# Kernel optimization log

Measured on AMD Instinct MI355X. Metric: run time of the kernel, lower is better.

## Reference

```python
import jax, jax.numpy as jnp
import numpy as np

B, S, H, DH = 4, 2048, 16, 64
D = H * DH          # 1024
EXP = 2
FF_IN = EXP * D * 2  # 4096 (SwiGLU doubles)
FF_HID = EXP * D     # 2048
SCALE_BASE = 512
LN_EPS = 1e-5


def setup_inputs() -> dict:
    key = jax.random.key(0)
    ks = jax.random.split(key, 8)
    inp = {
        "q": jax.random.normal(ks[0], (B, S, D), jnp.float32),
        "k": jax.random.normal(ks[1], (B, S, D), jnp.float32),
        "v": jax.random.normal(ks[2], (B, S, D), jnp.float32),
        "Wqkv": jax.random.normal(ks[3], (D, 3 * D), jnp.float32) * (1.0 / np.sqrt(D)),
        "bqkv": jnp.zeros((3 * D,), jnp.float32),
        "q_scale": jnp.ones((DH,), jnp.float32),
        "k_scale": jnp.ones((DH,), jnp.float32),
        "ln_g": jnp.ones((D,), jnp.float32),
        "ln_b": jnp.zeros((D,), jnp.float32),
        "W1": jax.random.normal(ks[4], (D, FF_IN), jnp.float32) * (1.0 / np.sqrt(D)),
        "b1": jnp.zeros((FF_IN,), jnp.float32),
        "W2": jax.random.normal(ks[5], (FF_HID, D), jnp.float32) * (1.0 / np.sqrt(FF_HID)),
        "b2": jnp.zeros((D,), jnp.float32),
    }
    return inp


def rotate_half(x):
    x1, x2 = jnp.split(x, 2, axis=-1)
    return jnp.concatenate((-x2, x1), axis=-1)


def apply_rope(pos, t, scale):
    # pos: [S, DH], scale: [S, DH] (broadcast over [B, H, S, DH])
    return t * jnp.cos(pos) * scale + rotate_half(t) * jnp.sin(pos) * scale


def rotary_tables(seq_len):
    inv_freq = 1.0 / (10000.0 ** (jnp.arange(0, DH, 2, dtype=jnp.float32) / DH))
    t = jnp.arange(seq_len, dtype=jnp.float32)
    freqs = t[:, None] * inv_freq[None, :]            # [S, DH/2]
    freqs = jnp.concatenate((freqs, freqs), axis=-1)  # [S, DH]
    power = (t - seq_len // 2) / SCALE_BASE           # [S]
    base = (jnp.arange(0, DH, 2, dtype=jnp.float32) + 0.4 * DH) / (1.4 * DH)  # [DH/2]
    scale = base[None, :] ** power[:, None]           # [S, DH/2]
    scale = jnp.concatenate((scale, scale), axis=-1)  # [S, DH]
    return freqs, scale


def l2norm(x, eps=1e-12):
    n = jnp.sqrt(jnp.sum(x * x, axis=-1, keepdims=True))
    return x / jnp.maximum(n, eps)


def reference(q, k, v, Wqkv, bqkv, q_scale, k_scale, ln_g, ln_b, W1, b1, W2, b2):
    del k, v  # module projects qkv from q; k,v args are unused (faithful to source)
    n, seq_len, _ = q.shape
    qkv = q @ Wqkv + bqkv                              # [B, S, 3D]
    qkv = qkv.reshape(n, seq_len, H, 3 * DH).transpose(0, 2, 1, 3)  # [B, H, S, 3DH]
    q_, k_, v_ = jnp.split(qkv, 3, axis=-1)
    q_ = l2norm(q_) * q_scale
    k_ = l2norm(k_) * k_scale
    pos, xscale = rotary_tables(seq_len)
    q_ = apply_rope(pos, q_, xscale)
    k_ = apply_rope(pos, k_, 1.0 / xscale)
    # scaled dot product attention (non-causal)
    scores = jnp.einsum("bhid,bhjd->bhij", q_, k_) / np.sqrt(DH)
    attn = jax.nn.softmax(scores, axis=-1)
    out = jnp.einsum("bhij,bhjd->bhid", attn, v_)      # [B, H, S, DH]
    out = out.transpose(0, 2, 1, 3).reshape(n, seq_len, D)
    # LayerNorm
    mu = jnp.mean(out, axis=-1, keepdims=True)
    var = jnp.mean((out - mu) ** 2, axis=-1, keepdims=True)
    out = (out - mu) / jnp.sqrt(var + LN_EPS) * ln_g + ln_b
    # SwiGLU FFN (dropout = identity in eval)
    h = out @ W1 + b1                                  # [B, S, FF_IN]
    x_, gate = jnp.split(h, 2, axis=-1)
    ff = (jax.nn.silu(gate) * x_) @ W2 + b2            # [B, S, D]
    return out + ff
```

## Files before the change

kernel.cpp:

```cpp
#include <hip/hip_runtime.h>
#include <math.h>


typedef __bf16 bf16;
typedef bf16 bf16x8 __attribute__((ext_vector_type(8)));
typedef bf16 bf16x4 __attribute__((ext_vector_type(4)));
typedef float f32x4 __attribute__((ext_vector_type(4)));

#define MFMA(a, b, c) __builtin_amdgcn_mfma_f32_16x16x32_bf16(a, b, c, 0, 0, 0)

__device__ __forceinline__ void async16(const void* g, void* l) {
    __builtin_amdgcn_global_load_lds(
        (const __attribute__((address_space(1))) void*)g,
        (__attribute__((address_space(3))) void*)l,
        16, 0, 0);
}

__global__ __launch_bounds__(256) void fill_sentinel(float* __restrict__ o)
{
    size_t i = ((size_t)blockIdx.x * 256 + threadIdx.x) * 4;
    *(float4*)&o[i] = make_float4(0.25f, 0.25f, 0.25f, 0.25f);
}

__global__ __launch_bounds__(256) void transpose_f32_bf16(
    const float* __restrict__ in, bf16* __restrict__ out, int K, int N)
{
    __shared__ bf16 T[64][70];
    const int tN = N >> 6;
    const int tk = blockIdx.x / tN, tn = blockIdx.x % tN;
    const int k0 = tk << 6, n0 = tn << 6;
    const int t = threadIdx.x;
    const int r = t >> 2, c0 = (t & 3) << 4;
    const float* src = &in[(size_t)(k0 + r) * N + n0 + c0];
    for (int j = 0; j < 4; ++j) {
        float4 f = *(const float4*)(src + 4 * j);
        T[r][c0 + 4 * j + 0] = (bf16)f.x;
        T[r][c0 + 4 * j + 1] = (bf16)f.y;
        T[r][c0 + 4 * j + 2] = (bf16)f.z;
        T[r][c0 + 4 * j + 3] = (bf16)f.w;
    }
    __syncthreads();
    bf16x8 o0, o1;
    for (int i = 0; i < 8; ++i) o0[i] = T[c0 + i][r];
    for (int i = 0; i < 8; ++i) o1[i] = T[c0 + 8 + i][r];
    *(bf16x8*)&out[(size_t)(n0 + r) * K + k0 + c0]     = o0;
    *(bf16x8*)&out[(size_t)(n0 + r) * K + k0 + c0 + 8] = o1;
}

__global__ __launch_bounds__(256) void transpose_v(
    const bf16* __restrict__ in, bf16* __restrict__ out)
{
    __shared__ bf16 T[64][72];
    const int bh = blockIdx.x >> 5;
    const int s0 = (blockIdx.x & 31) << 6;
    const bf16* ip = in + ((size_t)bh << 17) + (size_t)s0 * 64;
    bf16* op = out + ((size_t)bh << 17) + s0;
    const int t = threadIdx.x;
    const int r = t >> 2, c0 = (t & 3) << 4;
    *(bf16x8*)&T[r][c0]     = *(const bf16x8*)&ip[r * 64 + c0];
    *(bf16x8*)&T[r][c0 + 8] = *(const bf16x8*)&ip[r * 64 + c0 + 8];
    __syncthreads();
    bf16x8 o0, o1;
    for (int i = 0; i < 8; ++i) o0[i] = T[c0 + i][r];
    for (int i = 0; i < 8; ++i) o1[i] = T[c0 + 8 + i][r];
    *(bf16x8*)&op[(size_t)r * 2048 + c0]     = o0;
    *(bf16x8*)&op[(size_t)r * 2048 + c0 + 8] = o1;
}

template <int EPI, bool AF32>
__global__ __launch_bounds__(256) void gemm_bt(
    const void* __restrict__ Avp, const bf16* __restrict__ BT,
    const float* __restrict__ bias, int M, int N, int K, int lda,
    bf16* __restrict__ C0, bf16* __restrict__ C1, bf16* __restrict__ C2,
    float* __restrict__ Cf, const bf16* __restrict__ resid)
{
    __shared__ bf16 As[128 * 64];
    __shared__ bf16 Bs[128 * 64];
    const int tid = threadIdx.x;
    const int lane = tid & 63, wave = tid >> 6;
    const int quad = lane >> 4, l16 = lane & 15;
    const int wm = wave >> 1, wn = wave & 1;
    const int nb = N >> 7;
    const int bm = blockIdx.x / nb, bn = blockIdx.x % nb;
    const int m0 = bm << 7, n0 = bn << 7;
    const float* Af = (const float*)Avp;
    const bf16*  Ab = (const bf16*)Avp;
    char* aB = (char*)&As[0];
    char* bB = (char*)&Bs[0];
    const int rsw = l16 & 7;

    f32x4 acc[4][4] = {};

    for (int kt = 0; kt < K; kt += 64) {
        for (int i = 0; i < 4; ++i) {
            int l = (i << 8) + tid;
            int r = l >> 3;
            int cbs = ((l & 7) ^ (r & 7)) << 3;
            int cu = (i << 8) + (wave << 6);
            if (!AF32)
                async16(&Ab[(size_t)(m0 + r) * lda + kt + cbs], aB + (size_t)cu * 16);
            async16(&BT[(size_t)(n0 + r) * K + kt + cbs], bB + (size_t)cu * 16);
        }
        if (AF32) {
            for (int i = 0; i < 4; ++i) {
                int l = (i << 8) + tid;
                int r = l >> 3;
                int cbs = ((l & 7) ^ (r & 7)) << 3;
                const float* s = &Af[(size_t)(m0 + r) * lda + kt + cbs];
                float4 f0 = *(const float4*)s;
                float4 f1 = *(const float4*)(s + 4);
                bf16x8 tv;
                tv[0] = (bf16)f0.x; tv[1] = (bf16)f0.y;
                tv[2] = (bf16)f0.z; tv[3] = (bf16)f0.w;
                tv[4] = (bf16)f1.x; tv[5] = (bf16)f1.y;
                tv[6] = (bf16)f1.z; tv[7] = (bf16)f1.w;
                *(bf16x8*)&As[l << 3] = tv;
            }
        }
        __syncthreads();
        for (int kd = 0; kd < 2; ++kd) {
            bf16x8 af[4], bfr[4];
            for (int mi = 0; mi < 4; ++mi) {
                int row = (wm << 6) + (mi << 4) + l16;
                af[mi] = *(const bf16x8*)&As[(row << 6) + ((((kd << 2) + quad) ^ rsw) << 3)];
            }
            for (int ni = 0; ni < 4; ++ni) {
                int row = (wn << 6) + (ni << 4) + l16;
                bfr[ni] = *(const bf16x8*)&Bs[(row << 6) + ((((kd << 2) + quad) ^ rsw) << 3)];
            }
            for (int mi = 0; mi < 4; ++mi)
                for (int ni = 0; ni < 4; ++ni)
                    acc[mi][ni] = MFMA(af[mi], bfr[ni], acc[mi][ni]);
        }
        __syncthreads();
    }

    for (int mi = 0; mi < 4; ++mi) {
        for (int ni = 0; ni < 4; ++ni) {
            for (int r = 0; r < 4; ++r) {
                int row = m0 + (wm << 6) + (mi << 4) + (quad << 2) + r;
                int col = n0 + (wn << 6) + (ni << 4) + l16;
                float v = acc[mi][ni][r] + bias[col];
                if (EPI == 0) {
                    int b = row >> 11, s = row & 2047;
                    int h = col / 192, w = col % 192;
                    int tq = w >> 6, d = w & 63;
                    bf16* dst = (tq == 0) ? C0 : (tq == 1) ? C1 : C2;
                    dst[((((size_t)b * 16 + h) * 2048 + s) << 6) + d] = (bf16)v;
                } else if (EPI == 1) {
                    C0[(size_t)row * N + col] = (bf16)v;
                } else {
                    float rv = (float)resid[(size_t)row * N + col];
                    Cf[(size_t)row * N + col] = v + rv;
                }
            }
        }
    }
}

__global__ __launch_bounds__(256) void norm_rope(
    bf16* __restrict__ qb, bf16* __restrict__ kb,
    const float* __restrict__ qs, const float* __restrict__ ks)
{
    const int wave = threadIdx.x >> 6, lane = threadIdx.x & 63;
    const int rid = blockIdx.x * 4 + wave;
    const bool is_k = rid >= 131072;
    const int idx = is_k ? rid - 131072 : rid;
    const int s = idx & 2047;
    bf16* ptr = (is_k ? kb : qb) + ((size_t)idx << 6);
    const int d = lane;

    float v = (float)ptr[d];
    float ss = v * v;
    for (int o = 1; o < 64; o <<= 1) ss += __shfl_xor(ss, o);
    float t = v * rsqrtf(fmaxf(ss, 1e-24f));
    t *= (is_k ? ks : qs)[d];

    float partner = __shfl_xor(t, 32);
    float rh = (d < 32) ? -partner : partner;

    const float fi = (float)(d & 31);
    float inv_freq = __builtin_amdgcn_exp2f(fi * -0.4152410118609203f);
    float pos = (float)s * inv_freq;
    float rev = pos * 0.15915494309189535f;
    rev = rev - floorf(rev);
    float sn = __builtin_amdgcn_sinf(rev);
    float cs = __builtin_amdgcn_cosf(rev);
    float base = (2.0f * fi + 25.6f) * (1.0f / 89.6f);
    float power = ((float)s - 1024.0f) * (1.0f / 512.0f);
    if (is_k) power = -power;
    float xsc = __builtin_amdgcn_exp2f(power * __builtin_amdgcn_logf(base));
    ptr[d] = (bf16)((t * cs + rh * sn) * xsc);
}

__device__ __forceinline__ void attn_stage(
    const bf16* __restrict__ Kp, const bf16* __restrict__ Vp, int kt,
    char* kB, char* vB, int tid, int wave)
{
    for (int i = 0; i < 2; ++i) {
        int l = (i << 8) + tid;
        int r = l >> 3;
        int cbs = ((l & 7) ^ (r & 7)) << 3;
        int cu = (i << 8) + (wave << 6);
        async16(&Kp[(size_t)(kt + r) * 64 + cbs], kB + (size_t)cu * 16);
        async16(&Vp[(size_t)r * 2048 + kt + cbs], vB + (size_t)cu * 16);
    }
}

__global__ __launch_bounds__(256) void attn(
    const bf16* __restrict__ Q, const bf16* __restrict__ Kb,
    const bf16* __restrict__ VT, bf16* __restrict__ O)
{
    __shared__ bf16 Ks[2][64 * 64];
    __shared__ bf16 Vt[2][64 * 64];
    __shared__ bf16 Ps[4][2][16][72];
    const int tid = threadIdx.x;
    const int lane = tid & 63, wave = tid >> 6;
    const int quad = lane >> 4, l16 = lane & 15;
    const int rsw = l16 & 7;
    const int bh = blockIdx.x >> 4;
    const int q0 = (blockIdx.x & 15) << 7;
    const int s_base = q0 + (wave << 5);
    const bf16* Qp = Q + ((size_t)bh << 17);
    const bf16* Kp = Kb + ((size_t)bh << 17);
    const bf16* Vp = VT + ((size_t)bh << 17);

    bf16x8 qf[2][2];
    for (int sub = 0; sub < 2; ++sub) {
        const bf16* qrow = Qp + (size_t)(s_base + (sub << 4) + l16) * 64;
        qf[sub][0] = *(const bf16x8*)&qrow[(quad << 3)];
        qf[sub][1] = *(const bf16x8*)&qrow[32 + (quad << 3)];
        for (int j = 0; j < 8; ++j) {
            qf[sub][0][j] = (bf16)((float)qf[sub][0][j] * 0.1803368801f);
            qf[sub][1][j] = (bf16)((float)qf[sub][1][j] * 0.1803368801f);
        }
    }
    bf16x8 ones = {};
    if (l16 == 0) for (int j = 0; j < 8; ++j) ones[j] = (bf16)1.0f;

    f32x4 oacc[2][4] = {};
    f32x4 lacc[2] = {};

    attn_stage(Kp, Vp, 0, (char*)&Ks[0][0], (char*)&Vt[0][0], tid, wave);

    int buf = 0;
    for (int kt = 0; kt < 2048; kt += 64, buf ^= 1) {
        __syncthreads();
        if (kt + 64 < 2048)
            attn_stage(Kp, Vp, kt + 64,
                       (char*)&Ks[buf ^ 1][0], (char*)&Vt[buf ^ 1][0], tid, wave);

        const bf16* Kt_ = &Ks[buf][0];
        const bf16* Vc_ = &Vt[buf][0];

        f32x4 sc[2][4];
        __builtin_amdgcn_s_setprio(1);
        for (int nt = 0; nt < 4; ++nt) {
            int row = (nt << 4) + l16;
            bf16x8 kf0 = *(const bf16x8*)&Kt_[(row << 6) + ((quad ^ rsw) << 3)];
            bf16x8 kf1 = *(const bf16x8*)&Kt_[(row << 6) + (((quad + 4) ^ rsw) << 3)];
            for (int sub = 0; sub < 2; ++sub) {
                f32x4 z = {};
                z = MFMA(kf0, qf[sub][0], z);
                z = MFMA(kf1, qf[sub][1], z);
                sc[sub][nt] = z;
            }
        }
        __builtin_amdgcn_s_setprio(0);

        for (int sub = 0; sub < 2; ++sub)
            for (int nt = 0; nt < 4; ++nt) {
                bf16x4 pk;
                for (int r = 0; r < 4; ++r)
                    pk[r] = (bf16)__builtin_amdgcn_exp2f(sc[sub][nt][r]);
                *(bf16x4*)&Ps[wave][sub][l16][(nt << 4) + (quad << 2)] = pk;
            }
        __builtin_amdgcn_wave_barrier();
        bf16x8 pf0[2], pf1[2];
        for (int sub = 0; sub < 2; ++sub) {
            pf0[sub] = *(const bf16x8*)&Ps[wave][sub][l16][(quad << 3)];
            pf1[sub] = *(const bf16x8*)&Ps[wave][sub][l16][32 + (quad << 3)];
        }

        __builtin_amdgcn_s_setprio(1);
        for (int ntd = 0; ntd < 4; ++ntd) {
            int row = (ntd << 4) + l16;
            bf16x8 vf0 = *(const bf16x8*)&Vc_[(row << 6) + ((quad ^ rsw) << 3)];
            bf16x8 vf1 = *(const bf16x8*)&Vc_[(row << 6) + (((quad + 4) ^ rsw) << 3)];
            for (int sub = 0; sub < 2; ++sub) {
                oacc[sub][ntd] = MFMA(pf0[sub], vf0, oacc[sub][ntd]);
                oacc[sub][ntd] = MFMA(pf1[sub], vf1, oacc[sub][ntd]);
            }
        }
        for (int sub = 0; sub < 2; ++sub) {
            lacc[sub] = MFMA(pf0[sub], ones, lacc[sub]);
            lacc[sub] = MFMA(pf1[sub], ones, lacc[sub]);
        }
        __builtin_amdgcn_s_setprio(0);
    }

    const int b = bh >> 4, h = bh & 15;
    for (int sub = 0; sub < 2; ++sub)
        for (int r = 0; r < 4; ++r) {
            float l = __shfl(lacc[sub][r], quad << 4);
            float inv_l = 1.0f / l;
            int srow = s_base + (sub << 4) + (quad << 2) + r;
            for (int ntd = 0; ntd < 4; ++ntd) {
                int d = (ntd << 4) + l16;
                O[((((size_t)b * 2048 + srow) * 16) + h) * 64 + d] =
                    (bf16)(oacc[sub][ntd][r] * inv_l);
            }
        }
}

__global__ __launch_bounds__(256) void layernorm(
    const bf16* __restrict__ x, const float* __restrict__ g,
    const float* __restrict__ b, bf16* __restrict__ y)
{
    __shared__ float red[8];
    const int row = blockIdx.x;
    const int t = threadIdx.x;
    const bf16* xr = x + ((size_t)row << 10);
    bf16x4 xv = *(const bf16x4*)&xr[t << 2];
    float v[4], s = 0.0f, sq = 0.0f;
    for (int i = 0; i < 4; ++i) { v[i] = (float)xv[i]; s += v[i]; sq += v[i] * v[i]; }
    for (int o = 1; o < 64; o <<= 1) { s += __shfl_xor(s, o); sq += __shfl_xor(sq, o); }
    const int wave = t >> 6, lane = t & 63;
    if (lane == 0) { red[wave] = s; red[4 + wave] = sq; }
    __syncthreads();
    s  = red[0] + red[1] + red[2] + red[3];
    sq = red[4] + red[5] + red[6] + red[7];
    float mu = s * (1.0f / 1024.0f);
    float var = fmaxf(sq * (1.0f / 1024.0f) - mu * mu, 0.0f);
    float rstd = rsqrtf(var + 1e-5f);
    bf16x4 ov;
    for (int i = 0; i < 4; ++i) {
        int c = (t << 2) + i;
        ov[i] = (bf16)((v[i] - mu) * rstd * g[c] + b[c]);
    }
    *(bf16x4*)(y + ((size_t)row << 10) + (t << 2)) = ov;
}

__global__ __launch_bounds__(256) void swiglu(bf16* __restrict__ h)
{
    size_t i = ((size_t)blockIdx.x * 256 + threadIdx.x) * 8;
    size_t row = i >> 11, c = i & 2047;
    bf16* hr = h + (row << 12);
    bf16x8 xv = *(const bf16x8*)&hr[c];
    bf16x8 gv = *(const bf16x8*)&hr[c + 2048];
    bf16x8 ov;
    for (int j = 0; j < 8; ++j) {
        float xf = (float)xv[j], gf = (float)gv[j];
        ov[j] = (bf16)(gf / (1.0f + __expf(-gf)) * xf);
    }
    *(bf16x8*)&hr[c] = ov;
}

extern "C" void kernel_launch(void* const* d_in, const int* in_sizes, int n_in,
                              void* d_out, int out_size, void* d_ws, size_t ws_size,
                              hipStream_t stream) {
    (void)in_sizes; (void)n_in; (void)out_size;
    const float* q    = (const float*)d_in[0];
    const float* Wqkv = (const float*)d_in[3];
    const float* bqkv = (const float*)d_in[4];
    const float* qsc  = (const float*)d_in[5];
    const float* ksc  = (const float*)d_in[6];
    const float* lng  = (const float*)d_in[7];
    const float* lnb  = (const float*)d_in[8];
    const float* W1   = (const float*)d_in[9];
    const float* b1   = (const float*)d_in[10];
    const float* W2   = (const float*)d_in[11];
    const float* b2   = (const float*)d_in[12];
    float* out = (float*)d_out;

    const size_t MB = 1024 * 1024;
    if (ws_size < 92 * MB) {
        fill_sentinel<<<8192, 256, 0, stream>>>(out);
        return;
    }

    char* ws = (char*)d_ws;
    bf16* W2T      = (bf16*)(ws + 0);
    bf16* ln_buf   = (bf16*)(ws + 4  * MB);
    bf16* W1T      = (bf16*)(ws + 20 * MB);
    bf16* q_buf    = (bf16*)(ws + 28 * MB);
    bf16* k_buf    = (bf16*)(ws + 44 * MB);
    bf16* v_buf    = (bf16*)(ws + 60 * MB);
    bf16* WqkvT    = (bf16*)(ws + 76 * MB);
    bf16* vt_buf   = (bf16*)(ws + 76 * MB);
    bf16* attn_buf = (bf16*)(ws + 60 * MB);
    bf16* h_buf    = (bf16*)(ws + 28 * MB);

    transpose_f32_bf16<<<512,  256, 0, stream>>>(W2,   W2T,   2048, 1024);
    transpose_f32_bf16<<<1024, 256, 0, stream>>>(W1,   W1T,   1024, 4096);
    transpose_f32_bf16<<<768,  256, 0, stream>>>(Wqkv, WqkvT, 1024, 3072);

    gemm_bt<0, true><<<1536, 256, 0, stream>>>(q, WqkvT, bqkv, 8192, 3072, 1024, 1024,
                                               q_buf, k_buf, v_buf, nullptr, nullptr);
    norm_rope<<<65536, 256, 0, stream>>>(q_buf, k_buf, qsc, ksc);
    transpose_v<<<2048, 256, 0, stream>>>(v_buf, vt_buf);
    attn<<<1024, 256, 0, stream>>>(q_buf, k_buf, vt_buf, attn_buf);
    layernorm<<<8192, 256, 0, stream>>>(attn_buf, lng, lnb, ln_buf);
    gemm_bt<1, false><<<2048, 256, 0, stream>>>(ln_buf, W1T, b1, 8192, 4096, 1024, 1024,
                                                h_buf, nullptr, nullptr, nullptr, nullptr);
    swiglu<<<8192, 256, 0, stream>>>(h_buf);
    gemm_bt<2, false><<<512, 256, 0, stream>>>(h_buf, W2T, b2, 8192, 1024, 2048, 4096,
                                               nullptr, nullptr, nullptr, out, ln_buf);
}
```

Baseline: 540.5 us.

## Add 256x256 double-buffered async-LDS GEMM for QKV and W1 projections

Adds a new GEMM kernel with 256x256 output tiles, 512 threads, XOR-swizzled LDS, double-buffered global_load_lds staging and a grid swizzle. It replaces the 128x128 GEMM for the QKV and W1 projections. The fp32 input q is first converted to bf16 by a separate kernel so the new GEMM can stream bf16 directly. This aims to raise data reuse and MFMA utilization, at the cost of an extra conversion pass and heavier register and LDS use per block, which may limit occupancy.

```diff
diff --git a/kernel.cpp b/kernel.cpp
--- a/kernel.cpp
+++ b/kernel.cpp
@@ -20,6 +20,18 @@
 {
     size_t i = ((size_t)blockIdx.x * 256 + threadIdx.x) * 4;
     *(float4*)&o[i] = make_float4(0.25f, 0.25f, 0.25f, 0.25f);
+}
+
+__global__ __launch_bounds__(256) void convert_f32_bf16(
+    const float* __restrict__ in, bf16* __restrict__ out)
+{
+    size_t i = ((size_t)blockIdx.x * 256 + threadIdx.x) * 8;
+    float4 f0 = *(const float4*)&in[i];
+    float4 f1 = *(const float4*)&in[i + 4];
+    bf16x8 v;
+    v[0] = (bf16)f0.x; v[1] = (bf16)f0.y; v[2] = (bf16)f0.z; v[3] = (bf16)f0.w;
+    v[4] = (bf16)f1.x; v[5] = (bf16)f1.y; v[6] = (bf16)f1.z; v[7] = (bf16)f1.w;
+    *(bf16x8*)&out[i] = v;
 }
 
 __global__ __launch_bounds__(256) void transpose_f32_bf16(
@@ -65,6 +77,117 @@
     for (int i = 0; i < 8; ++i) o1[i] = T[c0 + 8 + i][r];
     *(bf16x8*)&op[(size_t)r * 2048 + c0]     = o0;
     *(bf16x8*)&op[(size_t)r * 2048 + c0 + 8] = o1;
+}
+
+__device__ __forceinline__ void g256_stage(
+    const bf16* __restrict__ Ag, const bf16* __restrict__ Bg, int kt, int K,
+    char* aB, char* bB, int tid, int wave)
+{
+    for (int i = 0; i < 4; ++i) {
+        int l = (i << 9) + tid;
+        int r = l >> 3;
+        int cbs = ((l & 7) ^ (r & 7)) << 3;
+        int cu = (i << 9) + (wave << 6);
+        async16(&Ag[(size_t)r * K + kt + cbs], aB + (size_t)cu * 16);
+        async16(&Bg[(size_t)r * K + kt + cbs], bB + (size_t)cu * 16);
+    }
+}
+
+__device__ __forceinline__ void g256_compute(
+    const bf16* At, const bf16* Bt, f32x4 (&acc)[8][4],
+    int wm, int wn, int l16, int quad, int rsw)
+{
+    for (int kd = 0; kd < 2; ++kd) {
+        bf16x8 af[8], bfr[4];
+        for (int mi = 0; mi < 8; ++mi) {
+            int row = (wm << 7) + (mi << 4) + l16;
+            af[mi] = *(const bf16x8*)&At[(row << 6) + ((((kd << 2) + quad) ^ rsw) << 3)];
+        }
+        for (int ni = 0; ni < 4; ++ni) {
+            int row = (wn << 6) + (ni << 4) + l16;
+            bfr[ni] = *(const bf16x8*)&Bt[(row << 6) + ((((kd << 2) + quad) ^ rsw) << 3)];
+        }
+        __builtin_amdgcn_s_setprio(1);
+        for (int mi = 0; mi < 8; ++mi)
+            for (int ni = 0; ni < 4; ++ni)
+                acc[mi][ni] = MFMA(af[mi], bfr[ni], acc[mi][ni]);
+        __builtin_amdgcn_s_setprio(0);
+    }
+}
+
+template <int EPI>
+__global__ __launch_bounds__(512, 2) void gemm256(
+    const bf16* __restrict__ A, const bf16* __restrict__ BT,
+    const float* __restrict__ bias, int M, int N, int K,
+    bf16* __restrict__ C0, bf16* __restrict__ C1, bf16* __restrict__ C2)
+{
+    __shared__ bf16 As[2][256 * 64];
+    __shared__ bf16 Bs[2][256 * 64];
+    const int tid = threadIdx.x;
+    const int lane = tid & 63, wave = tid >> 6;
+    const int quad = lane >> 4, l16 = lane & 15;
+    const int rsw = l16 & 7;
+    const int wm = wave >> 2, wn = wave & 3;
+    const int nb = N >> 8;
+    const int nwg = gridDim.x;
+    const int bid = blockIdx.x;
+    const int swz = (bid & 7) * (nwg >> 3) + (bid >> 3);
+    const int bm = swz / nb, bn = swz % nb;
+    const int m0 = bm << 8, n0 = bn << 8;
+    const bf16* Ag = A + (size_t)m0 * K;
+    const bf16* Bg = BT + (size_t)n0 * K;
+    char* a0 = (char*)&As[0][0]; char* a1 = (char*)&As[1][0];
+    char* b0 = (char*)&Bs[0][0]; char* b1 = (char*)&Bs[1][0];
+
+    f32x4 acc[8][4] = {};
+    const int NT = K >> 6;
+
+    g256_stage(Ag, Bg, 0,  K, a0, b0, tid, wave);
+    g256_stage(Ag, Bg, 64, K, a1, b1, tid, wave);
+    asm volatile("s_waitcnt vmcnt(8)" ::: "memory");
+    __builtin_amdgcn_s_barrier();
+
+    for (int t = 0; t < NT; t += 2) {
+        g256_compute(&As[0][0], &Bs[0][0], acc, wm, wn, l16, quad, rsw);
+        asm volatile("" ::: "memory");
+        __builtin_amdgcn_s_barrier();
+        if (t + 2 < NT) {
+            g256_stage(Ag, Bg, (t + 2) << 6, K, a0, b0, tid, wave);
+            asm volatile("s_waitcnt vmcnt(8)" ::: "memory");
+        } else {
+            asm volatile("s_waitcnt vmcnt(0)" ::: "memory");
+        }
+        __builtin_amdgcn_s_barrier();
+        g256_compute(&As[1][0], &Bs[1][0], acc, wm, wn, l16, quad, rsw);
+        asm volatile("" ::: "memory");
+        __builtin_amdgcn_s_barrier();
+        if (t + 3 < NT) {
+            g256_stage(Ag, Bg, (t + 3) << 6, K, a1, b1, tid, wave);
+            asm volatile("s_waitcnt vmcnt(8)" ::: "memory");
+        } else {
+            asm volatile("s_waitcnt vmcnt(0)" ::: "memory");
+        }
+        __builtin_amdgcn_s_barrier();
+    }
+
+    for (int mi = 0; mi < 8; ++mi) {
+        for (int ni = 0; ni < 4; ++ni) {
+            for (int r = 0; r < 4; ++r) {
+                int row = m0 + (wm << 7) + (mi << 4) + (quad << 2) + r;
+                int col = n0 + (wn << 6) + (ni << 4) + l16;
+                float v = acc[mi][ni][r] + bias[col];
+                if (EPI == 0) {
+                    int b = row >> 11, s = row & 2047;
+                    int h = col / 192, w = col % 192;
+                    int tq = w >> 6, d = w & 63;
+                    bf16* dst = (tq == 0) ? C0 : (tq == 1) ? C1 : C2;
+                    dst[((((size_t)b * 16 + h) * 2048 + s) << 6) + d] = (bf16)v;
+                } else {
+                    C0[(size_t)row * N + col] = (bf16)v;
+                }
+            }
+        }
+    }
 }
 
 template <int EPI, bool AF32>
@@ -382,6 +505,7 @@
     char* ws = (char*)d_ws;
     bf16* W2T      = (bf16*)(ws + 0);
     bf16* ln_buf   = (bf16*)(ws + 4  * MB);
+    bf16* q_bf     = (bf16*)(ws + 4  * MB);
     bf16* W1T      = (bf16*)(ws + 20 * MB);
     bf16* q_buf    = (bf16*)(ws + 28 * MB);
     bf16* k_buf    = (bf16*)(ws + 44 * MB);
@@ -391,18 +515,19 @@
     bf16* attn_buf = (bf16*)(ws + 60 * MB);
     bf16* h_buf    = (bf16*)(ws + 28 * MB);
 
+    convert_f32_bf16<<<4096, 256, 0, stream>>>(q, q_bf);
     transpose_f32_bf16<<<512,  256, 0, stream>>>(W2,   W2T,   2048, 1024);
     transpose_f32_bf16<<<1024, 256, 0, stream>>>(W1,   W1T,   1024, 4096);
     transpose_f32_bf16<<<768,  256, 0, stream>>>(Wqkv, WqkvT, 1024, 3072);
 
-    gemm_bt<0, true><<<1536, 256, 0, stream>>>(q, WqkvT, bqkv, 8192, 3072, 1024, 1024,
-                                               q_buf, k_buf, v_buf, nullptr, nullptr);
+    gemm256<0><<<384, 512, 0, stream>>>(q_bf, WqkvT, bqkv, 8192, 3072, 1024,
+                                        q_buf, k_buf, v_buf);
     norm_rope<<<65536, 256, 0, stream>>>(q_buf, k_buf, qsc, ksc);
     transpose_v<<<2048, 256, 0, stream>>>(v_buf, vt_buf);
     attn<<<1024, 256, 0, stream>>>(q_buf, k_buf, vt_buf, attn_buf);
     layernorm<<<8192, 256, 0, stream>>>(attn_buf, lng, lnb, ln_buf);
-    gemm_bt<1, false><<<2048, 256, 0, stream>>>(ln_buf, W1T, b1, 8192, 4096, 1024, 1024,
-                                                h_buf, nullptr, nullptr, nullptr, nullptr);
+    gemm256<1><<<512, 512, 0, stream>>>(ln_buf, W1T, b1, 8192, 4096, 1024,
+                                        h_buf, nullptr, nullptr);
     swiglu<<<8192, 256, 0, stream>>>(h_buf);
     gemm_bt<2, false><<<512, 256, 0, stream>>>(h_buf, W2T, b2, 8192, 1024, 2048, 4096,
                                                nullptr, nullptr, nullptr, out, ln_buf);
```

After: 509.7 us. 5.7% less time.

## Replace GEMMs with 256-row double-buffered 512-thread tiles and swizzle attention P buffer

Applied to the files above, without the earlier changes.

Replaces the 128x128 single-buffered GEMM with a 256xBN tile kernel using 8 waves, double-buffered async LDS loads with explicit vmcnt waits, block-index swizzling for L2 locality, and raised MFMA priority. The fp32 input q is now converted to bf16 in a separate pass so the QKV GEMM can use async loads as well. The attention P scratch buffer drops its padding and uses an XOR swizzle to avoid bank conflicts. Larger tiles increase per-block register and LDS pressure, and the bigger tiles produce fewer blocks, which could hurt occupancy or the tail.

```diff
diff --git a/kernel.cpp b/kernel.cpp
--- a/kernel.cpp
+++ b/kernel.cpp
@@ -20,6 +20,18 @@
 {
     size_t i = ((size_t)blockIdx.x * 256 + threadIdx.x) * 4;
     *(float4*)&o[i] = make_float4(0.25f, 0.25f, 0.25f, 0.25f);
+}
+
+__global__ __launch_bounds__(256) void convert_f32_bf16(
+    const float* __restrict__ in, bf16* __restrict__ out)
+{
+    size_t i = ((size_t)blockIdx.x * 256 + threadIdx.x) * 8;
+    float4 f0 = *(const float4*)&in[i];
+    float4 f1 = *(const float4*)&in[i + 4];
+    bf16x8 v;
+    v[0] = (bf16)f0.x; v[1] = (bf16)f0.y; v[2] = (bf16)f0.z; v[3] = (bf16)f0.w;
+    v[4] = (bf16)f1.x; v[5] = (bf16)f1.y; v[6] = (bf16)f1.z; v[7] = (bf16)f1.w;
+    *(bf16x8*)&out[i] = v;
 }
 
 __global__ __launch_bounds__(256) void transpose_f32_bf16(
@@ -67,79 +79,116 @@
     *(bf16x8*)&op[(size_t)r * 2048 + c0 + 8] = o1;
 }
 
-template <int EPI, bool AF32>
-__global__ __launch_bounds__(256) void gemm_bt(
-    const void* __restrict__ Avp, const bf16* __restrict__ BT,
+template <int BN>
+__device__ __forceinline__ void g256_stage(
+    const bf16* __restrict__ Ag, const bf16* __restrict__ Bg, int kt,
+    int lda, int K, char* aB, char* bB, int tid, int wave)
+{
+    for (int i = 0; i < 4; ++i) {
+        int l = (i << 9) + tid;
+        int r = l >> 3;
+        int cbs = ((l & 7) ^ (r & 7)) << 3;
+        int cu = (i << 9) + (wave << 6);
+        async16(&Ag[(size_t)r * lda + kt + cbs], aB + (size_t)cu * 16);
+    }
+    for (int i = 0; i < BN / 64; ++i) {
+        int l = (i << 9) + tid;
+        int r = l >> 3;
+        int cbs = ((l & 7) ^ (r & 7)) << 3;
+        int cu = (i << 9) + (wave << 6);
+        async16(&Bg[(size_t)r * K + kt + cbs], bB + (size_t)cu * 16);
+    }
+}
+
+template <int NI>
+__device__ __forceinline__ void g256_compute(
+    const bf16* At, const bf16* Bt, f32x4 (&acc)[8][NI],
+    int wm, int wn, int l16, int quad, int rsw)
+{
+    for (int kd = 0; kd < 2; ++kd) {
+        bf16x8 af[8], bfr[NI];
+        for (int mi = 0; mi < 8; ++mi) {
+            int row = (wm << 7) + (mi << 4) + l16;
+            af[mi] = *(const bf16x8*)&At[(row << 6) + ((((kd << 2) + quad) ^ rsw) << 3)];
+        }
+        for (int ni = 0; ni < NI; ++ni) {
+            int row = wn * (NI << 4) + (ni << 4) + l16;
+            bfr[ni] = *(const bf16x8*)&Bt[(row << 6) + ((((kd << 2) + quad) ^ rsw) << 3)];
+        }
+        __builtin_amdgcn_s_setprio(1);
+        for (int mi = 0; mi < 8; ++mi)
+            for (int ni = 0; ni < NI; ++ni)
+                acc[mi][ni] = MFMA(af[mi], bfr[ni], acc[mi][ni]);
+        __builtin_amdgcn_s_setprio(0);
+    }
+}
+
+#define G256_WAIT()                                                        \
+    if constexpr (BN == 256) asm volatile("s_waitcnt vmcnt(8)" ::: "memory"); \
+    else                     asm volatile("s_waitcnt vmcnt(6)" ::: "memory")
+
+template <int EPI, int BN>
+__global__ __launch_bounds__(512, 2) void gemm256(
+    const bf16* __restrict__ A, const bf16* __restrict__ BT,
     const float* __restrict__ bias, int M, int N, int K, int lda,
     bf16* __restrict__ C0, bf16* __restrict__ C1, bf16* __restrict__ C2,
     float* __restrict__ Cf, const bf16* __restrict__ resid)
 {
-    __shared__ bf16 As[128 * 64];
-    __shared__ bf16 Bs[128 * 64];
+    constexpr int NI = BN / 64;
+    __shared__ bf16 As[2][256 * 64];
+    __shared__ bf16 Bs[2][BN * 64];
     const int tid = threadIdx.x;
     const int lane = tid & 63, wave = tid >> 6;
     const int quad = lane >> 4, l16 = lane & 15;
-    const int wm = wave >> 1, wn = wave & 1;
-    const int nb = N >> 7;
-    const int bm = blockIdx.x / nb, bn = blockIdx.x % nb;
-    const int m0 = bm << 7, n0 = bn << 7;
-    const float* Af = (const float*)Avp;
-    const bf16*  Ab = (const bf16*)Avp;
-    char* aB = (char*)&As[0];
-    char* bB = (char*)&Bs[0];
     const int rsw = l16 & 7;
-
-    f32x4 acc[4][4] = {};
-
-    for (int kt = 0; kt < K; kt += 64) {
-        for (int i = 0; i < 4; ++i) {
-            int l = (i << 8) + tid;
-            int r = l >> 3;
-            int cbs = ((l & 7) ^ (r & 7)) << 3;
-            int cu = (i << 8) + (wave << 6);
-            if (!AF32)
-                async16(&Ab[(size_t)(m0 + r) * lda + kt + cbs], aB + (size_t)cu * 16);
-            async16(&BT[(size_t)(n0 + r) * K + kt + cbs], bB + (size_t)cu * 16);
-        }
-        if (AF32) {
-            for (int i = 0; i < 4; ++i) {
-                int l = (i << 8) + tid;
-                int r = l >> 3;
-                int cbs = ((l & 7) ^ (r & 7)) << 3;
-                const float* s = &Af[(size_t)(m0 + r) * lda + kt + cbs];
-                float4 f0 = *(const float4*)s;
-                float4 f1 = *(const float4*)(s + 4);
-                bf16x8 tv;
-                tv[0] = (bf16)f0.x; tv[1] = (bf16)f0.y;
-                tv[2] = (bf16)f0.z; tv[3] = (bf16)f0.w;
-                tv[4] = (bf16)f1.x; tv[5] = (bf16)f1.y;
-                tv[6] = (bf16)f1.z; tv[7] = (bf16)f1.w;
-                *(bf16x8*)&As[l << 3] = tv;
-            }
-        }
-        __syncthreads();
-        for (int kd = 0; kd < 2; ++kd) {
-            bf16x8 af[4], bfr[4];
-            for (int mi = 0; mi < 4; ++mi) {
-                int row = (wm << 6) + (mi << 4) + l16;
-                af[mi] = *(const bf16x8*)&As[(row << 6) + ((((kd << 2) + quad) ^ rsw) << 3)];
-            }
-            for (int ni = 0; ni < 4; ++ni) {
-                int row = (wn << 6) + (ni << 4) + l16;
-                bfr[ni] = *(const bf16x8*)&Bs[(row << 6) + ((((kd << 2) + quad) ^ rsw) << 3)];
-            }
-            for (int mi = 0; mi < 4; ++mi)
-                for (int ni = 0; ni < 4; ++ni)
-                    acc[mi][ni] = MFMA(af[mi], bfr[ni], acc[mi][ni]);
-        }
-        __syncthreads();
-    }
-
-    for (int mi = 0; mi < 4; ++mi) {
-        for (int ni = 0; ni < 4; ++ni) {
+    const int wm = wave >> 2, wn = wave & 3;
+    const int nb = N / BN;
+    const int nwg = gridDim.x;
+    const int bid = blockIdx.x;
+    const int swz = (bid & 7) * (nwg >> 3) + (bid >> 3);
+    const int bm = swz / nb, bn = swz % nb;
+    const int m0 = bm << 8, n0 = bn * BN;
+    const bf16* Ag = A + (size_t)m0 * lda;
+    const bf16* Bg = BT + (size_t)n0 * K;
+    char* a0 = (char*)&As[0][0]; char* a1 = (char*)&As[1][0];
+    char* b0 = (char*)&Bs[0][0]; char* b1 = (char*)&Bs[1][0];
+
+    f32x4 acc[8][NI] = {};
+    const int NT = K >> 6;
+
+    g256_stage<BN>(Ag, Bg, 0,  lda, K, a0, b0, tid, wave);
+    g256_stage<BN>(Ag, Bg, 64, lda, K, a1, b1, tid, wave);
+    G256_WAIT();
+    __builtin_amdgcn_s_barrier();
+
+    for (int t = 0; t < NT; t += 2) {
+        g256_compute<NI>(&As[0][0], &Bs[0][0], acc, wm, wn, l16, quad, rsw);
+        asm volatile("" ::: "memory");
+        __builtin_amdgcn_s_barrier();
+        if (t + 2 < NT) {
+            g256_stage<BN>(Ag, Bg, (t + 2) << 6, lda, K, a0, b0, tid, wave);
+            G256_WAIT();
+        } else {
+            asm volatile("s_waitcnt vmcnt(0)" ::: "memory");
+        }
+        __builtin_amdgcn_s_barrier();
+        g256_compute<NI>(&As[1][0], &Bs[1][0], acc, wm, wn, l16, quad, rsw);
+        asm volatile("" ::: "memory");
+        __builtin_amdgcn_s_barrier();
+        if (t + 3 < NT) {
+            g256_stage<BN>(Ag, Bg, (t + 3) << 6, lda, K, a1, b1, tid, wave);
+            G256_WAIT();
+        } else {
+            asm volatile("s_waitcnt vmcnt(0)" ::: "memory");
+        }
+        __builtin_amdgcn_s_barrier();
+    }
+
+    for (int mi = 0; mi < 8; ++mi) {
+        for (int ni = 0; ni < NI; ++ni) {
             for (int r = 0; r < 4; ++r) {
-                int row = m0 + (wm << 6) + (mi << 4) + (quad << 2) + r;
-                int col = n0 + (wn << 6) + (ni << 4) + l16;
+                int row = m0 + (wm << 7) + (mi << 4) + (quad << 2) + r;
+                int col = n0 + wn * (NI << 4) + (ni << 4) + l16;
                 float v = acc[mi][ni][r] + bias[col];
                 if (EPI == 0) {
                     int b = row >> 11, s = row & 2047;
@@ -213,7 +262,7 @@
 {
     __shared__ bf16 Ks[2][64 * 64];
     __shared__ bf16 Vt[2][64 * 64];
-    __shared__ bf16 Ps[4][2][16][72];
+    __shared__ bf16 Ps[4][2][16][64];
     const int tid = threadIdx.x;
     const int lane = tid & 63, wave = tid >> 6;
     const int quad = lane >> 4, l16 = lane & 15;
@@ -273,13 +322,13 @@
                 bf16x4 pk;
                 for (int r = 0; r < 4; ++r)
                     pk[r] = (bf16)__builtin_amdgcn_exp2f(sc[sub][nt][r]);
-                *(bf16x4*)&Ps[wave][sub][l16][(nt << 4) + (quad << 2)] = pk;
+                *(bf16x4*)&Ps[wave][sub][l16][(((nt << 2) + quad) ^ (rsw << 1)) << 2] = pk;
             }
         __builtin_amdgcn_wave_barrier();
         bf16x8 pf0[2], pf1[2];
         for (int sub = 0; sub < 2; ++sub) {
-            pf0[sub] = *(const bf16x8*)&Ps[wave][sub][l16][(quad << 3)];
-            pf1[sub] = *(const bf16x8*)&Ps[wave][sub][l16][32 + (quad << 3)];
+            pf0[sub] = *(const bf16x8*)&Ps[wave][sub][l16][(quad ^ rsw) << 3];
+            pf1[sub] = *(const bf16x8*)&Ps[wave][sub][l16][((quad + 4) ^ rsw) << 3];
         }
 
         __builtin_amdgcn_s_setprio(1);
@@ -382,6 +431,7 @@
     char* ws = (char*)d_ws;
     bf16* W2T      = (bf16*)(ws + 0);
     bf16* ln_buf   = (bf16*)(ws + 4  * MB);
+    bf16* q_bf     = (bf16*)(ws + 4  * MB);
     bf16* W1T      = (bf16*)(ws + 20 * MB);
     bf16* q_buf    = (bf16*)(ws + 28 * MB);
     bf16* k_buf    = (bf16*)(ws + 44 * MB);
@@ -391,19 +441,20 @@
     bf16* attn_buf = (bf16*)(ws + 60 * MB);
     bf16* h_buf    = (bf16*)(ws + 28 * MB);
 
+    convert_f32_bf16<<<4096, 256, 0, stream>>>(q, q_bf);
     transpose_f32_bf16<<<512,  256, 0, stream>>>(W2,   W2T,   2048, 1024);
     transpose_f32_bf16<<<1024, 256, 0, stream>>>(W1,   W1T,   1024, 4096);
     transpose_f32_bf16<<<768,  256, 0, stream>>>(Wqkv, WqkvT, 1024, 3072);
 
-    gemm_bt<0, true><<<1536, 256, 0, stream>>>(q, WqkvT, bqkv, 8192, 3072, 1024, 1024,
-                                               q_buf, k_buf, v_buf, nullptr, nullptr);
+    gemm256<0, 128><<<768, 512, 0, stream>>>(q_bf, WqkvT, bqkv, 8192, 3072, 1024, 1024,
+                                             q_buf, k_buf, v_buf, nullptr, nullptr);
     norm_rope<<<65536, 256, 0, stream>>>(q_buf, k_buf, qsc, ksc);
     transpose_v<<<2048, 256, 0, stream>>>(v_buf, vt_buf);
     attn<<<1024, 256, 0, stream>>>(q_buf, k_buf, vt_buf, attn_buf);
     layernorm<<<8192, 256, 0, stream>>>(attn_buf, lng, lnb, ln_buf);
-    gemm_bt<1, false><<<2048, 256, 0, stream>>>(ln_buf, W1T, b1, 8192, 4096, 1024, 1024,
-                                                h_buf, nullptr, nullptr, nullptr, nullptr);
+    gemm256<1, 256><<<512, 512, 0, stream>>>(ln_buf, W1T, b1, 8192, 4096, 1024, 1024,
+                                             h_buf, nullptr, nullptr, nullptr, nullptr);
     swiglu<<<8192, 256, 0, stream>>>(h_buf);
-    gemm_bt<2, false><<<512, 256, 0, stream>>>(h_buf, W2T, b2, 8192, 1024, 2048, 4096,
-                                               nullptr, nullptr, nullptr, out, ln_buf);
-}
+    gemm256<2, 128><<<256, 512, 0, stream>>>(h_buf, W2T, b2, 8192, 1024, 2048, 4096,
+                                             nullptr, nullptr, nullptr, out, ln_buf);
+}
```

Measured after the change: 515.4 us. -4.6%, faster.
